# Optimization experiments

Measured on AMD Instinct MI355X. Metric: run time of the kernel, lower is better.

The kernel has to match this reference:

```python
import jax, jax.numpy as jnp
import numpy as np

B, W, S, D, H = 16, 128, 16, 768, 12
HD = D // H

def _ln(x, g, b):
    m = x.mean(-1, keepdims=True)
    v = ((x - m) ** 2).mean(-1, keepdims=True)
    return (x - m) / jnp.sqrt(v + 1e-5) * g + b

def _lin(x, w, b):
    return x @ w.T + b

def _rope(t):
    # t: (N, H, L, HD); interleaved even/odd rotation, base 10000
    inv = 1.0 / (10000.0 ** (jnp.arange(0, HD, 2, dtype=jnp.float32) / HD))
    fr = jnp.arange(t.shape[2], dtype=jnp.float32)[:, None] * inv[None, :]  # (L, HD//2)
    cos, sin = jnp.cos(fr), jnp.sin(fr)
    te, to = t[..., ::2], t[..., 1::2]
    return jnp.stack([te * cos - to * sin, te * sin + to * cos], -1).reshape(t.shape)

def _mha(q, k, v, mask=None):
    # q,k,v: (N, H, L, HD)
    s = jnp.einsum('nhqd,nhkd->nhqk', q, k) / jnp.sqrt(jnp.float32(HD))
    if mask is not None:
        s = jnp.where(mask[None, None], -jnp.inf, s)
    a = jax.nn.softmax(s, axis=-1)
    return jnp.einsum('nhqk,nhkd->nhqd', a, v)

def _heads(t, L):
    return t.reshape(-1, L, H, HD).transpose(0, 2, 1, 3)

def setup_inputs() -> dict:
    key = jax.random.key(0)
    ks = jax.random.split(key, 16)
    def w(i, shape):
        return jax.random.normal(ks[i], shape, jnp.float32) * 0.02
    return {
        'x': jax.random.normal(ks[0], (B, W, S, D), jnp.float32),
        'causal_mask': jnp.triu(jnp.ones((W, W), dtype=bool), k=1),
        'sn_g': jnp.ones((D,), jnp.float32), 'sn_b': jnp.zeros((D,), jnp.float32),
        'sa_in_w': w(1, (3 * D, D)), 'sa_in_b': jnp.zeros((3 * D,), jnp.float32),
        'sa_out_w': w(2, (D, D)), 'sa_out_b': jnp.zeros((D,), jnp.float32),
        'tn_g': jnp.ones((D,), jnp.float32), 'tn_b': jnp.zeros((D,), jnp.float32),
        'tq_w': w(3, (D, D)), 'tq_b': jnp.zeros((D,), jnp.float32),
        'tk_w': w(4, (D, D)), 'tk_b': jnp.zeros((D,), jnp.float32),
        'tv_w': w(5, (D, D)), 'tv_b': jnp.zeros((D,), jnp.float32),
        'to_w': w(6, (D, D)), 'to_b': jnp.zeros((D,), jnp.float32),
        'fn_g': jnp.ones((D,), jnp.float32), 'fn_b': jnp.zeros((D,), jnp.float32),
        'f1_w': w(7, (4 * D, D)), 'f1_b': jnp.zeros((4 * D,), jnp.float32),
        'f2_w': w(8, (D, 4 * D)), 'f2_b': jnp.zeros((D,), jnp.float32),
    }

def reference(x, causal_mask, sn_g, sn_b, sa_in_w, sa_in_b, sa_out_w, sa_out_b,
              tn_g, tn_b, tq_w, tq_b, tk_w, tk_b, tv_w, tv_b, to_w, to_b,
              fn_g, fn_b, f1_w, f1_b, f2_w, f2_b):
    # ---- spatial attention within each timestep: (B*W, S, D) ----
    xs = x.reshape(B * W, S, D)
    xn = _ln(xs, sn_g, sn_b)
    q, k, v = jnp.split(_lin(xn, sa_in_w, sa_in_b), 3, axis=-1)
    o = _mha(_heads(q, S), _heads(k, S), _heads(v, S))
    o = o.transpose(0, 2, 1, 3).reshape(B * W, S, D)
    xs = xs + _lin(o, sa_out_w, sa_out_b)
    x = xs.reshape(B, W, S, D)
    # ---- causal temporal attention with RoPE: (B*S, W, D) ----
    xt = x.transpose(0, 2, 1, 3).reshape(B * S, W, D)
    xn = _ln(xt, tn_g, tn_b)
    q = _rope(_heads(_lin(xn, tq_w, tq_b), W))
    k = _rope(_heads(_lin(xn, tk_w, tk_b), W))
    v = _heads(_lin(xn, tv_w, tv_b), W)
    o = _mha(q, k, v, causal_mask)
    o = o.transpose(0, 2, 1, 3).reshape(B * S, W, D)
    xt = xt + _lin(o, to_w, to_b)
    x = xt.reshape(B, S, W, D).transpose(0, 2, 1, 3)
    # ---- feed-forward (exact GELU, as torch default) ----
    h = jax.nn.gelu(_lin(_ln(x, fn_g, fn_b), f1_w, f1_b), approximate=False)
    return x + _lin(h, f2_w, f2_b)
```

## Files before the change

### kernel.cpp

```cpp
#include <hip/hip_runtime.h>
#include <stdint.h>


#define NB 16
#define NW 128
#define NS 16
#define ND 768
#define NH 12
#define NTOK 32768

typedef __attribute__((ext_vector_type(8))) short short8;
typedef __attribute__((ext_vector_type(4))) float f32x4;

__device__ __forceinline__ float blo(unsigned v){ return __builtin_bit_cast(float, v << 16); }
__device__ __forceinline__ float bhi(unsigned v){ return __builtin_bit_cast(float, v & 0xffff0000u); }
__device__ __forceinline__ float bus(unsigned short u){ return __builtin_bit_cast(float, ((unsigned)u) << 16); }
__device__ __forceinline__ unsigned short f2b(float f){
  unsigned u = __builtin_bit_cast(unsigned, f);
  u += 0x7fffu + ((u >> 16) & 1u);
  return (unsigned short)(u >> 16);
}
__device__ __forceinline__ void gld_lds16(const void* g, void* l){
  __builtin_amdgcn_global_load_lds((const __attribute__((address_space(1))) void*)g,
                                   (__attribute__((address_space(3))) void*)l, 16, 0, 0);
}

__global__ __launch_bounds__(256) void convert_k(const float* __restrict__ in,
                                                 unsigned short* __restrict__ out, int n4){
  int i = blockIdx.x * 256 + threadIdx.x;
  int stride = gridDim.x * 256;
  for (; i < n4; i += stride){
    float4 v = ((const float4*)in)[i];
    unsigned lo = (unsigned)f2b(v.x) | ((unsigned)f2b(v.y) << 16);
    unsigned hi = (unsigned)f2b(v.z) | ((unsigned)f2b(v.w) << 16);
    ((uint2*)out)[i] = make_uint2(lo, hi);
  }
}

__global__ __launch_bounds__(256) void concat3_k(const float* __restrict__ a, const float* __restrict__ b,
                                                 const float* __restrict__ c, float* __restrict__ o){
  int i = blockIdx.x * 256 + threadIdx.x;
  if (i < 768){ o[i] = a[i]; o[768 + i] = b[i]; o[1536 + i] = c[i]; }
}

__global__ __launch_bounds__(256) void rope_k(float* __restrict__ tab){
  int i = blockIdx.x * 256 + threadIdx.x;
  if (i < 128 * 32){
    int w = i >> 5, p = i & 31;
    float inv = powf(10000.0f, -((float)(2 * p)) / 64.0f);
    float ang = (float)w * inv;
    tab[i * 2] = cosf(ang);
    tab[i * 2 + 1] = sinf(ang);
  }
}

template<int INF32>
__global__ __launch_bounds__(256) void ln_k(const void* __restrict__ xin, const float* __restrict__ g,
                                            const float* __restrict__ bt, unsigned short* __restrict__ out){
  const int row = blockIdx.x;
  const int t = threadIdx.x;
  const float* xf = (const float*)xin;
  const unsigned short* xb = (const unsigned short*)xin;
  float v[3];
#pragma unroll
  for (int i = 0; i < 3; ++i){
    int j = t + i * 256;
    v[i] = INF32 ? xf[(size_t)row * 768 + j] : bus(xb[(size_t)row * 768 + j]);
  }
  float s = v[0] + v[1] + v[2];
  float ss = v[0]*v[0] + v[1]*v[1] + v[2]*v[2];
#pragma unroll
  for (int o = 1; o < 64; o <<= 1){ s += __shfl_xor(s, o, 64); ss += __shfl_xor(ss, o, 64); }
  __shared__ float red[8];
  int w = t >> 6;
  if ((t & 63) == 0){ red[w*2] = s; red[w*2+1] = ss; }
  __syncthreads();
  s = red[0] + red[2] + red[4] + red[6];
  ss = red[1] + red[3] + red[5] + red[7];
  float mean = s * (1.0f / 768.0f);
  float var = ss * (1.0f / 768.0f) - mean * mean;
  float rstd = rsqrtf(var + 1e-5f);
#pragma unroll
  for (int i = 0; i < 3; ++i){
    int j = t + i * 256;
    out[(size_t)row * 768 + j] = f2b((v[i] - mean) * rstd * g[j] + bt[j]);
  }
}

template<int MODE, int MROWS>
__global__ __launch_bounds__(512) void gemm256_k(const unsigned short* __restrict__ A,
                                                 const unsigned short* __restrict__ Bw,
                                                 const float* __restrict__ bias,
                                                 const void* __restrict__ resid,
                                                 void* __restrict__ outp, int K, int M){
  constexpr int MH = MROWS / 2;
  constexpr int ASH = (MROWS == 8) ? 14 : 13;
  constexpr int NJA = MROWS / 4;
  constexpr int LDSZ = 4 * (1 << ASH) + 65536;
  __shared__ char LB[LDSZ];
  char* const Asl = LB;
  char* const Bsl = LB + 4 * (1 << ASH);
  const int tid = threadIdx.x;
  const int lane = tid & 63, w = tid >> 6;
  const int llo = lane & 15, lhi = lane >> 4;
  const int wm = w >> 2, wn = w & 3;
  const int NT = K >> 6;

  const int gx = gridDim.x;
  const int nwg = gx * gridDim.y;
  const int orig = blockIdx.y * gx + blockIdx.x;
  const int lin = (nwg & 7) ? orig : ((orig & 7) * (nwg >> 3) + (orig >> 3));
  const int by = lin / gx, bx = lin - by * gx;
  const int brow = by * (MROWS << 5);
  const int bcol = bx << 8;

  const int r0 = tid >> 3, cp = tid & 7;
  const int swz = (cp << 4) ^ ((r0 & 7) << 4);
  const char* aG = (const char*)(A + (size_t)(brow + r0) * K) + swz;
  const char* bG = (const char*)(Bw + (size_t)(bcol + r0) * K) + swz;
  const int J  = K * 128;
  const int Ha = K * (MROWS << 5);
  const int Hb = K * 256;
  const int ldst = w << 10;

  auto stage_a = [&](int gb, char* slotbase){
    gld_lds16(aG + gb, slotbase + ldst);
    if constexpr (NJA == 2) gld_lds16(aG + gb + J, slotbase + ldst + (1 << 13));
  };
  auto stage_b = [&](int gb, char* slotbase){
    gld_lds16(bG + gb, slotbase + ldst);
    gld_lds16(bG + gb + J, slotbase + ldst + (1 << 13));
  };

  stage_a(0,        Asl);
  stage_a(Ha,       Asl + (1 << ASH));
  stage_b(0,        Bsl);
  stage_b(Hb,       Bsl + (1 << 14));
  stage_a(128,      Asl + (2 << ASH));
  stage_a(128 + Ha, Asl + (3 << ASH));
  if constexpr (NJA == 2) asm volatile("s_waitcnt vmcnt(4)" ::: "memory");
  else                    asm volatile("s_waitcnt vmcnt(2)" ::: "memory");
  __builtin_amdgcn_s_barrier();

  f32x4 acc[MROWS][4];
#pragma unroll
  for (int m = 0; m < MROWS; ++m)
#pragma unroll
    for (int n = 0; n < 4; ++n) acc[m][n] = f32x4{0.f, 0.f, 0.f, 0.f};

  for (int t = 0; t < NT; ++t){
    const char* Ab = Asl + (((2 * t + wm) & 3) << ASH);
    const char* Bb = Bsl + (((2 * t + (wn >> 1)) & 3) << 14);
    const int tb = t << 7;
    short8 a0[MH][2], a1[MH][2], b0[2][2], b1[2][2];

#pragma unroll
    for (int ni = 0; ni < 2; ++ni){
      const int cc = ((wn & 1) << 6) + (ni << 4) + llo;
#pragma unroll
      for (int ks = 0; ks < 2; ++ks)
        b0[ni][ks] = *(const short8*)(Bb + cc * 128 + (((ks << 6) + (lhi << 4)) ^ ((cc & 7) << 4)));
    }
#pragma unroll
    for (int mi = 0; mi < MH; ++mi){
      const int rr = (mi << 4) + llo;
#pragma unroll
      for (int ks = 0; ks < 2; ++ks)
        a0[mi][ks] = *(const short8*)(Ab + rr * 128 + (((ks << 6) + (lhi << 4)) ^ ((rr & 7) << 4)));
    }
    if (t + 1 < NT) stage_b(tb + 128, Bsl + (((2 * t + 2) & 3) << 14));
    __builtin_amdgcn_s_barrier();
    __builtin_amdgcn_s_setprio(1);
#pragma unroll
    for (int mi = 0; mi < MH; ++mi)
#pragma unroll
      for (int ni = 0; ni < 2; ++ni){
        acc[mi][ni] = __builtin_amdgcn_mfma_f32_16x16x32_bf16(b0[ni][0], a0[mi][0], acc[mi][ni], 0, 0, 0);
        acc[mi][ni] = __builtin_amdgcn_mfma_f32_16x16x32_bf16(b0[ni][1], a0[mi][1], acc[mi][ni], 0, 0, 0);
      }
    __builtin_amdgcn_s_setprio(0);
    __builtin_amdgcn_s_barrier();

#pragma unroll
    for (int mi = 0; mi < MH; ++mi){
      const int rr = (MH << 4) + (mi << 4) + llo;
#pragma unroll
      for (int ks = 0; ks < 2; ++ks)
        a1[mi][ks] = *(const short8*)(Ab + rr * 128 + (((ks << 6) + (lhi << 4)) ^ ((rr & 7) << 4)));
    }
#pragma unroll
    for (int ni = 0; ni < 2; ++ni){
      const int cc = ((wn & 1) << 6) + 32 + (ni << 4) + llo;
#pragma unroll
      for (int ks = 0; ks < 2; ++ks)
        b1[ni][ks] = *(const short8*)(Bb + cc * 128 + (((ks << 6) + (lhi << 4)) ^ ((cc & 7) << 4)));
    }
    if (t + 1 < NT) stage_b(tb + 128 + Hb, Bsl + (((2 * t + 3) & 3) << 14));
    __builtin_amdgcn_s_barrier();
    __builtin_amdgcn_s_setprio(1);
#pragma unroll
    for (int mi = 0; mi < MH; ++mi)
#pragma unroll
      for (int ni = 0; ni < 2; ++ni){
        acc[MH + mi][ni] = __builtin_amdgcn_mfma_f32_16x16x32_bf16(b0[ni][0], a1[mi][0], acc[MH + mi][ni], 0, 0, 0);
        acc[MH + mi][ni] = __builtin_amdgcn_mfma_f32_16x16x32_bf16(b0[ni][1], a1[mi][1], acc[MH + mi][ni], 0, 0, 0);
      }
    __builtin_amdgcn_s_setprio(0);
    __builtin_amdgcn_s_barrier();

    if (t + 2 < NT) stage_a(tb + 256, Asl + (((2 * t + 4) & 3) << ASH));
    __builtin_amdgcn_s_barrier();
    __builtin_amdgcn_s_setprio(1);
#pragma unroll
    for (int mi = 0; mi < MH; ++mi)
#pragma unroll
      for (int ni = 0; ni < 2; ++ni){
        acc[mi][2 + ni] = __builtin_amdgcn_mfma_f32_16x16x32_bf16(b1[ni][0], a0[mi][0], acc[mi][2 + ni], 0, 0, 0);
        acc[mi][2 + ni] = __builtin_amdgcn_mfma_f32_16x16x32_bf16(b1[ni][1], a0[mi][1], acc[mi][2 + ni], 0, 0, 0);
      }
    __builtin_amdgcn_s_setprio(0);
    __builtin_amdgcn_s_barrier();

    if (t + 2 < NT) stage_a(tb + 256 + Ha, Asl + (((2 * t + 5) & 3) << ASH));
    __builtin_amdgcn_s_barrier();
    __builtin_amdgcn_s_setprio(1);
#pragma unroll
    for (int mi = 0; mi < MH; ++mi)
#pragma unroll
      for (int ni = 0; ni < 2; ++ni){
        acc[MH + mi][2 + ni] = __builtin_amdgcn_mfma_f32_16x16x32_bf16(b1[ni][0], a1[mi][0], acc[MH + mi][2 + ni], 0, 0, 0);
        acc[MH + mi][2 + ni] = __builtin_amdgcn_mfma_f32_16x16x32_bf16(b1[ni][1], a1[mi][1], acc[MH + mi][2 + ni], 0, 0, 0);
      }
    __builtin_amdgcn_s_setprio(0);
    if (t + 2 < NT){
      if constexpr (NJA == 2) asm volatile("s_waitcnt vmcnt(4)" ::: "memory");
      else                    asm volatile("s_waitcnt vmcnt(2)" ::: "memory");
    } else {
      asm volatile("s_waitcnt vmcnt(0)" ::: "memory");
    }
    __builtin_amdgcn_s_barrier();
  }

  const int orow = brow + wm * (MROWS << 4);
  const int ocol = bcol + (wn << 6);
  const unsigned short* resb = (const unsigned short*)resid;
  const float* resf = (const float*)resid;
#pragma unroll
  for (int m = 0; m < MROWS; ++m){
    const int row = orow + (m << 4) + llo;
    const size_t rb = (size_t)row * M;
#pragma unroll
    for (int n = 0; n < 4; ++n){
      const int col = ocol + (n << 4) + (lhi << 2);
      const float4 bv = *(const float4*)&bias[col];
      float v0 = acc[m][n][0] + bv.x;
      float v1 = acc[m][n][1] + bv.y;
      float v2 = acc[m][n][2] + bv.z;
      float v3 = acc[m][n][3] + bv.w;
      const size_t off = rb + col;
      if (MODE == 1){
        float y0 = v0 * (1.5957691216f + 0.0713548163f * v0 * v0);
        float y1 = v1 * (1.5957691216f + 0.0713548163f * v1 * v1);
        float y2 = v2 * (1.5957691216f + 0.0713548163f * v2 * v2);
        float y3 = v3 * (1.5957691216f + 0.0713548163f * v3 * v3);
        v0 = v0 / (1.0f + __expf(-y0));
        v1 = v1 / (1.0f + __expf(-y1));
        v2 = v2 / (1.0f + __expf(-y2));
        v3 = v3 / (1.0f + __expf(-y3));
      } else if (MODE == 2){
        const float4 rv = *(const float4*)&resf[off];
        v0 += rv.x; v1 += rv.y; v2 += rv.z; v3 += rv.w;
      } else if (MODE == 3 || MODE == 4){
        const uint2 rv = *(const uint2*)&resb[off];
        v0 += blo(rv.x); v1 += bhi(rv.x); v2 += blo(rv.y); v3 += bhi(rv.y);
      }
      if (MODE == 4){
        float4 ov; ov.x = v0; ov.y = v1; ov.z = v2; ov.w = v3;
        *(float4*)&((float*)outp)[off] = ov;
      } else {
        unsigned lo = (unsigned)f2b(v0) | ((unsigned)f2b(v1) << 16);
        unsigned hi = (unsigned)f2b(v2) | ((unsigned)f2b(v3) << 16);
        *(uint2*)&((unsigned short*)outp)[off] = make_uint2(lo, hi);
      }
    }
  }
}

__global__ __launch_bounds__(256) void sattn_k(const unsigned short* __restrict__ qkv,
                                               unsigned short* __restrict__ o){
  const int bw = blockIdx.x, h = blockIdx.y;
  const int t = threadIdx.x;
  __shared__ unsigned short qh[16 * 68], kh[16 * 68], vh[16 * 68];
  __shared__ float pl[16 * 17];
  const int row = t >> 4, c4 = t & 15;
  const size_t base = ((size_t)(bw * 16 + row)) * 2304 + h * 64 + c4 * 4;
  *(uint2*)&qh[row * 68 + c4 * 4] = *(const uint2*)&qkv[base];
  *(uint2*)&kh[row * 68 + c4 * 4] = *(const uint2*)&qkv[base + 768];
  *(uint2*)&vh[row * 68 + c4 * 4] = *(const uint2*)&qkv[base + 1536];
  __syncthreads();

  const int q = row, k = c4;
  float s = 0.f;
#pragma unroll
  for (int c = 0; c < 16; ++c){
    uint2 qv = *(const uint2*)&qh[q * 68 + c * 4];
    uint2 kv = *(const uint2*)&kh[k * 68 + c * 4];
    s += blo(qv.x) * blo(kv.x) + bhi(qv.x) * bhi(kv.x);
    s += blo(qv.y) * blo(kv.y) + bhi(qv.y) * bhi(kv.y);
  }
  s *= 0.125f;
  float m = s;
#pragma unroll
  for (int off = 1; off < 16; off <<= 1) m = fmaxf(m, __shfl_xor(m, off, 64));
  float p = __expf(s - m);
  float su = p;
#pragma unroll
  for (int off = 1; off < 16; off <<= 1) su += __shfl_xor(su, off, 64);
  pl[q * 17 + k] = p / su;
  __syncthreads();

  float o0 = 0.f, o1 = 0.f, o2 = 0.f, o3 = 0.f;
#pragma unroll
  for (int kk = 0; kk < 16; ++kk){
    float pw = pl[q * 17 + kk];
    uint2 vv = *(const uint2*)&vh[kk * 68 + c4 * 4];
    o0 += pw * blo(vv.x); o1 += pw * bhi(vv.x);
    o2 += pw * blo(vv.y); o3 += pw * bhi(vv.y);
  }
  const size_t ob = ((size_t)(bw * 16 + q)) * 768 + h * 64 + c4 * 4;
  unsigned r0 = (unsigned)f2b(o0) | ((unsigned)f2b(o1) << 16);
  unsigned r1 = (unsigned)f2b(o2) | ((unsigned)f2b(o3) << 16);
  *(uint2*)&o[ob] = make_uint2(r0, r1);
}

__global__ __launch_bounds__(256) void tattn_k(const unsigned short* __restrict__ qkv,
                                               const float* __restrict__ rope,
                                               unsigned short* __restrict__ o){
  const int bs = blockIdx.x, h = blockIdx.y;
  const int b = bs >> 4, s = bs & 15;
  const int t = threadIdx.x, lane = t & 63, w = t >> 6;
  const int lhi = lane >> 4, llo = lane & 15;
  __shared__ unsigned short Qs[128 * 64];
  __shared__ unsigned short Ks[128 * 64];
  __shared__ unsigned short Vt[64 * 128];
  __shared__ unsigned short P[128 * 128];

  {
    const int r = t >> 1;
    const int dbase = (t & 1) * 32;
    const size_t tokb = ((size_t)((b * 128 + r) * 16 + s)) * 2304 + h * 64;
    const float2* rp = (const float2*)rope;
#pragma unroll
    for (int mch = 0; mch < 4; ++mch){
      const int d0 = dbase + mch * 8;
      uint4 qv = *(const uint4*)&qkv[tokb + d0];
      uint4 kv = *(const uint4*)&qkv[tokb + 768 + d0];
      uint4 vv = *(const uint4*)&qkv[tokb + 1536 + d0];
      unsigned qin[4] = {qv.x, qv.y, qv.z, qv.w};
      unsigned kin[4] = {kv.x, kv.y, kv.z, kv.w};
      unsigned qo[4], ko[4];
#pragma unroll
      for (int j = 0; j < 4; ++j){
        float2 cssn = rp[r * 32 + (d0 >> 1) + j];
        float cs = cssn.x, sn = cssn.y;
        float qe = blo(qin[j]), qd = bhi(qin[j]);
        float ke = blo(kin[j]), kd = bhi(kin[j]);
        qo[j] = (unsigned)f2b(qe * cs - qd * sn) | ((unsigned)f2b(qe * sn + qd * cs) << 16);
        ko[j] = (unsigned)f2b(ke * cs - kd * sn) | ((unsigned)f2b(ke * sn + kd * cs) << 16);
      }
      const int byq = r * 128 + ((d0 * 2) ^ ((r & 7) << 4));
      *(uint4*)((char*)Qs + byq) = make_uint4(qo[0], qo[1], qo[2], qo[3]);
      *(uint4*)((char*)Ks + byq) = make_uint4(ko[0], ko[1], ko[2], ko[3]);
      unsigned vin[4] = {vv.x, vv.y, vv.z, vv.w};
#pragma unroll
      for (int j = 0; j < 8; ++j){
        const int d = d0 + j;
        unsigned short val = (j & 1) ? (unsigned short)(vin[j >> 1] >> 16)
                                     : (unsigned short)(vin[j >> 1] & 0xffffu);
        *(unsigned short*)((char*)Vt + d * 256 + ((r * 2) ^ ((d & 7) << 4))) = val;
      }
    }
  }
  __syncthreads();

  const int qbase = w * 32;
  f32x4 st[8][2];
#pragma unroll
  for (int i = 0; i < 8; ++i){ st[i][0] = f32x4{0.f,0.f,0.f,0.f}; st[i][1] = f32x4{0.f,0.f,0.f,0.f}; }
#pragma unroll
  for (int kd = 0; kd < 2; ++kd){
    short8 bq[2];
#pragma unroll
    for (int fq = 0; fq < 2; ++fq){
      const int qr = qbase + fq * 16 + llo;
      bq[fq] = *(const short8*)((const char*)Qs + qr * 128 + ((kd * 64 + lhi * 16) ^ ((qr & 7) << 4)));
    }
#pragma unroll
    for (int fk = 0; fk < 8; ++fk){
      const int kr = fk * 16 + llo;
      short8 ak = *(const short8*)((const char*)Ks + kr * 128 + ((kd * 64 + lhi * 16) ^ ((kr & 7) << 4)));
      st[fk][0] = __builtin_amdgcn_mfma_f32_16x16x32_bf16(ak, bq[0], st[fk][0], 0, 0, 0);
      st[fk][1] = __builtin_amdgcn_mfma_f32_16x16x32_bf16(ak, bq[1], st[fk][1], 0, 0, 0);
    }
  }

#pragma unroll
  for (int fq = 0; fq < 2; ++fq){
    const int qg = qbase + fq * 16 + llo;
    float m = -1e30f;
#pragma unroll
    for (int fk = 0; fk < 8; ++fk)
#pragma unroll
      for (int rr = 0; rr < 4; ++rr){
        const int kg = fk * 16 + lhi * 4 + rr;
        float sv = (kg <= qg) ? st[fk][fq][rr] : -1e30f;
        st[fk][fq][rr] = sv;
        m = fmaxf(m, sv);
      }
    m = fmaxf(m, __shfl_xor(m, 16, 64));
    m = fmaxf(m, __shfl_xor(m, 32, 64));
    float su = 0.f;
#pragma unroll
    for (int fk = 0; fk < 8; ++fk)
#pragma unroll
      for (int rr = 0; rr < 4; ++rr){
        float p = __expf((st[fk][fq][rr] - m) * 0.125f);
        st[fk][fq][rr] = p;
        su += p;
      }
    su += __shfl_xor(su, 16, 64);
    su += __shfl_xor(su, 32, 64);
    const float rs = 1.0f / su;
#pragma unroll
    for (int fk = 0; fk < 8; ++fk){
      const int kk = fk * 16 + lhi * 4;
      unsigned lo = (unsigned)f2b(st[fk][fq][0] * rs) | ((unsigned)f2b(st[fk][fq][1] * rs) << 16);
      unsigned hi = (unsigned)f2b(st[fk][fq][2] * rs) | ((unsigned)f2b(st[fk][fq][3] * rs) << 16);
      *(uint2*)((char*)P + qg * 256 + ((kk * 2) ^ ((qg & 7) << 4))) = make_uint2(lo, hi);
    }
  }
  __syncthreads();

  f32x4 oacc[2][4];
#pragma unroll
  for (int i = 0; i < 2; ++i)
#pragma unroll
    for (int j = 0; j < 4; ++j) oacc[i][j] = f32x4{0.f,0.f,0.f,0.f};
#pragma unroll
  for (int ks = 0; ks < 4; ++ks){
    short8 pa[2];
#pragma unroll
    for (int fq = 0; fq < 2; ++fq){
      const int qr = qbase + fq * 16 + llo;
      pa[fq] = *(const short8*)((const char*)P + qr * 256 + ((ks * 64 + lhi * 16) ^ ((qr & 7) << 4)));
    }
#pragma unroll
    for (int fd = 0; fd < 4; ++fd){
      const int dr = fd * 16 + llo;
      short8 vb = *(const short8*)((const char*)Vt + dr * 256 + ((ks * 64 + lhi * 16) ^ ((dr & 7) << 4)));
      oacc[0][fd] = __builtin_amdgcn_mfma_f32_16x16x32_bf16(pa[0], vb, oacc[0][fd], 0, 0, 0);
      oacc[1][fd] = __builtin_amdgcn_mfma_f32_16x16x32_bf16(pa[1], vb, oacc[1][fd], 0, 0, 0);
    }
  }

#pragma unroll
  for (int fq = 0; fq < 2; ++fq)
#pragma unroll
    for (int fd = 0; fd < 4; ++fd)
#pragma unroll
      for (int rr = 0; rr < 4; ++rr){
        const int qg = qbase + fq * 16 + lhi * 4 + rr;
        const int d = fd * 16 + llo;
        const size_t ob = ((size_t)((b * 128 + qg) * 16 + s)) * 768 + h * 64 + d;
        o[ob] = f2b(oacc[fq][fd][rr]);
      }
}

__global__ __launch_bounds__(256) void sentinel_k(float* out){
  if (blockIdx.x == 0 && threadIdx.x == 0) out[0] = 12345.0f;
}

extern "C" void kernel_launch(void* const* d_in, const int* in_sizes, int n_in,
                              void* d_out, int out_size, void* d_ws, size_t ws_size,
                              hipStream_t stream){
  const float* x       = (const float*)d_in[0];
  const float* sn_g    = (const float*)d_in[2];
  const float* sn_b    = (const float*)d_in[3];
  const float* sa_in_w = (const float*)d_in[4];
  const float* sa_in_b = (const float*)d_in[5];
  const float* sa_out_w= (const float*)d_in[6];
  const float* sa_out_b= (const float*)d_in[7];
  const float* tn_g    = (const float*)d_in[8];
  const float* tn_b    = (const float*)d_in[9];
  const float* tq_w    = (const float*)d_in[10];
  const float* tq_b    = (const float*)d_in[11];
  const float* tk_w    = (const float*)d_in[12];
  const float* tk_b    = (const float*)d_in[13];
  const float* tv_w    = (const float*)d_in[14];
  const float* tv_b    = (const float*)d_in[15];
  const float* to_w    = (const float*)d_in[16];
  const float* to_b    = (const float*)d_in[17];
  const float* fn_g    = (const float*)d_in[18];
  const float* fn_b    = (const float*)d_in[19];
  const float* f1_w    = (const float*)d_in[20];
  const float* f1_b    = (const float*)d_in[21];
  const float* f2_w    = (const float*)d_in[22];
  const float* f2_b    = (const float*)d_in[23];

  char* ws = (char*)d_ws;
  size_t off = 0;
  auto alloc = [&](size_t bytes) -> void* {
    void* p = ws + off;
    off += (bytes + 255) & ~(size_t)255;
    return p;
  };
  unsigned short* Wqkv = (unsigned short*)alloc((size_t)2304*768*2);
  unsigned short* Wo1  = (unsigned short*)alloc((size_t)768*768*2);
  unsigned short* W3   = (unsigned short*)alloc((size_t)2304*768*2);
  float*          b3   = (float*)alloc(2304*4);
  unsigned short* Wto  = (unsigned short*)alloc((size_t)768*768*2);
  unsigned short* Wf1  = (unsigned short*)alloc((size_t)3072*768*2);
  unsigned short* Wf2  = (unsigned short*)alloc((size_t)768*3072*2);
  float*          rope = (float*)alloc(128*32*2*4);
  unsigned short* xn   = (unsigned short*)alloc((size_t)NTOK*768*2);
  unsigned short* qkv  = (unsigned short*)alloc((size_t)NTOK*3072*2);
  unsigned short* xs2  = (unsigned short*)alloc((size_t)NTOK*768*2);
  unsigned short* xt2  = (unsigned short*)alloc((size_t)NTOK*768*2);
  unsigned short* ob   = xn;

  if (ws_size < off){ sentinel_k<<<1, 64, 0, stream>>>((float*)d_out); return; }

  convert_k<<<1024, 256, 0, stream>>>(sa_in_w, Wqkv, 2304*768/4);
  convert_k<<<512, 256, 0, stream>>>(sa_out_w, Wo1, 768*768/4);
  convert_k<<<512, 256, 0, stream>>>(tq_w, W3, 768*768/4);
  convert_k<<<512, 256, 0, stream>>>(tk_w, W3 + 768*768, 768*768/4);
  convert_k<<<512, 256, 0, stream>>>(tv_w, W3 + 2*768*768, 768*768/4);
  concat3_k<<<3, 256, 0, stream>>>(tq_b, tk_b, tv_b, b3);
  convert_k<<<512, 256, 0, stream>>>(to_w, Wto, 768*768/4);
  convert_k<<<1024, 256, 0, stream>>>(f1_w, Wf1, 3072*768/4);
  convert_k<<<1024, 256, 0, stream>>>(f2_w, Wf2, 768*3072/4);
  rope_k<<<16, 256, 0, stream>>>(rope);

  ln_k<1><<<NTOK, 256, 0, stream>>>(x, sn_g, sn_b, xn);
  gemm256_k<0,4><<<dim3(9, 256), 512, 0, stream>>>(xn, Wqkv, sa_in_b, nullptr, qkv, 768, 2304);
  sattn_k<<<dim3(2048, 12), 256, 0, stream>>>(qkv, ob);
  gemm256_k<2,4><<<dim3(3, 256), 512, 0, stream>>>(ob, Wo1, sa_out_b, x, xs2, 768, 768);

  ln_k<0><<<NTOK, 256, 0, stream>>>(xs2, tn_g, tn_b, xn);
  gemm256_k<0,4><<<dim3(9, 256), 512, 0, stream>>>(xn, W3, b3, nullptr, qkv, 768, 2304);
  tattn_k<<<dim3(256, 12), 256, 0, stream>>>(qkv, rope, ob);
  gemm256_k<3,4><<<dim3(3, 256), 512, 0, stream>>>(ob, Wto, to_b, xs2, xt2, 768, 768);

  ln_k<0><<<NTOK, 256, 0, stream>>>(xt2, fn_g, fn_b, xn);
  gemm256_k<1,8><<<dim3(12, 128), 512, 0, stream>>>(xn, Wf1, f1_b, nullptr, qkv, 768, 3072);
  gemm256_k<4,4><<<dim3(3, 256), 512, 0, stream>>>(qkv, Wf2, f2_b, xt2, d_out, 3072, 768);
}
```

Before: 1.129 ms.

## Prefetch next k-tile fragments from LDS and reorder GEMM phase schedule

Restructures the GEMM main loop so the a0/b0 register fragments for the next k-step are read from LDS before the last MFMA quadrant of the current step, and the a1/b1 reads are interleaved with earlier quadrants. The aim is to hide LDS read latency behind MFMA work and to drop one barrier phase per iteration. The cost is that the fragment registers now live across the loop, which raises register pressure, and the changed barrier and waitcnt ordering risks LDS slot hazards if any reuse window is wrong.

```diff
diff --git a/kernel.cpp b/kernel.cpp
--- a/kernel.cpp
+++ b/kernel.cpp
@@ -132,6 +132,44 @@
     gld_lds16(bG + gb + J, slotbase + ldst + (1 << 13));
   };
 
+  short8 a0[MH][2], a1[MH][2], b0[2][2], b1[2][2];
+  auto rd_a = [&](short8 (&dst)[MH][2], const char* Ab, int rbase){
+#pragma unroll
+    for (int mi = 0; mi < MH; ++mi){
+      const int rr = rbase + (mi << 4) + llo;
+#pragma unroll
+      for (int ks = 0; ks < 2; ++ks)
+        dst[mi][ks] = *(const short8*)(Ab + rr * 128 + (((ks << 6) + (lhi << 4)) ^ ((rr & 7) << 4)));
+    }
+  };
+  auto rd_b = [&](short8 (&dst)[2][2], const char* Bb, int cbase){
+#pragma unroll
+    for (int ni = 0; ni < 2; ++ni){
+      const int cc = cbase + (ni << 4) + llo;
+#pragma unroll
+      for (int ks = 0; ks < 2; ++ks)
+        dst[ni][ks] = *(const short8*)(Bb + cc * 128 + (((ks << 6) + (lhi << 4)) ^ ((cc & 7) << 4)));
+    }
+  };
+
+  f32x4 acc[MROWS][4];
+#pragma unroll
+  for (int m = 0; m < MROWS; ++m)
+#pragma unroll
+    for (int n = 0; n < 4; ++n) acc[m][n] = f32x4{0.f, 0.f, 0.f, 0.f};
+
+  auto mfma_q = [&](int mo, int no, short8 (&bb)[2][2], short8 (&aa)[MH][2]){
+    __builtin_amdgcn_s_setprio(1);
+#pragma unroll
+    for (int mi = 0; mi < MH; ++mi)
+#pragma unroll
+      for (int ni = 0; ni < 2; ++ni){
+        acc[mo + mi][no + ni] = __builtin_amdgcn_mfma_f32_16x16x32_bf16(bb[ni][0], aa[mi][0], acc[mo + mi][no + ni], 0, 0, 0);
+        acc[mo + mi][no + ni] = __builtin_amdgcn_mfma_f32_16x16x32_bf16(bb[ni][1], aa[mi][1], acc[mo + mi][no + ni], 0, 0, 0);
+      }
+    __builtin_amdgcn_s_setprio(0);
+  };
+
   stage_a(0,        Asl);
   stage_a(Ha,       Asl + (1 << ASH));
   stage_b(0,        Bsl);
@@ -141,103 +179,50 @@
   if constexpr (NJA == 2) asm volatile("s_waitcnt vmcnt(4)" ::: "memory");
   else                    asm volatile("s_waitcnt vmcnt(2)" ::: "memory");
   __builtin_amdgcn_s_barrier();
-
-  f32x4 acc[MROWS][4];
-#pragma unroll
-  for (int m = 0; m < MROWS; ++m)
-#pragma unroll
-    for (int n = 0; n < 4; ++n) acc[m][n] = f32x4{0.f, 0.f, 0.f, 0.f};
+  {
+    const char* Ab0 = Asl + ((wm & 3) << ASH);
+    const char* Bb0 = Bsl + (((wn >> 1) & 3) << 14);
+    rd_b(b0, Bb0, (wn & 1) << 6);
+    rd_a(a0, Ab0, 0);
+  }
 
   for (int t = 0; t < NT; ++t){
     const char* Ab = Asl + (((2 * t + wm) & 3) << ASH);
     const char* Bb = Bsl + (((2 * t + (wn >> 1)) & 3) << 14);
     const int tb = t << 7;
-    short8 a0[MH][2], a1[MH][2], b0[2][2], b1[2][2];
-
-#pragma unroll
-    for (int ni = 0; ni < 2; ++ni){
-      const int cc = ((wn & 1) << 6) + (ni << 4) + llo;
-#pragma unroll
-      for (int ks = 0; ks < 2; ++ks)
-        b0[ni][ks] = *(const short8*)(Bb + cc * 128 + (((ks << 6) + (lhi << 4)) ^ ((cc & 7) << 4)));
-    }
-#pragma unroll
-    for (int mi = 0; mi < MH; ++mi){
-      const int rr = (mi << 4) + llo;
-#pragma unroll
-      for (int ks = 0; ks < 2; ++ks)
-        a0[mi][ks] = *(const short8*)(Ab + rr * 128 + (((ks << 6) + (lhi << 4)) ^ ((rr & 7) << 4)));
-    }
+
+    rd_a(a1, Ab, MH << 4);
+    __builtin_amdgcn_s_barrier();
+    mfma_q(0, 0, b0, a0);
+    __builtin_amdgcn_s_barrier();
+
+    rd_b(b1, Bb, ((wn & 1) << 6) + 32);
     if (t + 1 < NT) stage_b(tb + 128, Bsl + (((2 * t + 2) & 3) << 14));
     __builtin_amdgcn_s_barrier();
-    __builtin_amdgcn_s_setprio(1);
-#pragma unroll
-    for (int mi = 0; mi < MH; ++mi)
-#pragma unroll
-      for (int ni = 0; ni < 2; ++ni){
-        acc[mi][ni] = __builtin_amdgcn_mfma_f32_16x16x32_bf16(b0[ni][0], a0[mi][0], acc[mi][ni], 0, 0, 0);
-        acc[mi][ni] = __builtin_amdgcn_mfma_f32_16x16x32_bf16(b0[ni][1], a0[mi][1], acc[mi][ni], 0, 0, 0);
-      }
-    __builtin_amdgcn_s_setprio(0);
-    __builtin_amdgcn_s_barrier();
-
-#pragma unroll
-    for (int mi = 0; mi < MH; ++mi){
-      const int rr = (MH << 4) + (mi << 4) + llo;
-#pragma unroll
-      for (int ks = 0; ks < 2; ++ks)
-        a1[mi][ks] = *(const short8*)(Ab + rr * 128 + (((ks << 6) + (lhi << 4)) ^ ((rr & 7) << 4)));
-    }
-#pragma unroll
-    for (int ni = 0; ni < 2; ++ni){
-      const int cc = ((wn & 1) << 6) + 32 + (ni << 4) + llo;
-#pragma unroll
-      for (int ks = 0; ks < 2; ++ks)
-        b1[ni][ks] = *(const short8*)(Bb + cc * 128 + (((ks << 6) + (lhi << 4)) ^ ((cc & 7) << 4)));
-    }
+    mfma_q(MH, 0, b0, a1);
+    __builtin_amdgcn_s_barrier();
+
     if (t + 1 < NT) stage_b(tb + 128 + Hb, Bsl + (((2 * t + 3) & 3) << 14));
-    __builtin_amdgcn_s_barrier();
-    __builtin_amdgcn_s_setprio(1);
-#pragma unroll
-    for (int mi = 0; mi < MH; ++mi)
-#pragma unroll
-      for (int ni = 0; ni < 2; ++ni){
-        acc[MH + mi][ni] = __builtin_amdgcn_mfma_f32_16x16x32_bf16(b0[ni][0], a1[mi][0], acc[MH + mi][ni], 0, 0, 0);
-        acc[MH + mi][ni] = __builtin_amdgcn_mfma_f32_16x16x32_bf16(b0[ni][1], a1[mi][1], acc[MH + mi][ni], 0, 0, 0);
-      }
-    __builtin_amdgcn_s_setprio(0);
-    __builtin_amdgcn_s_barrier();
-
     if (t + 2 < NT) stage_a(tb + 256, Asl + (((2 * t + 4) & 3) << ASH));
     __builtin_amdgcn_s_barrier();
-    __builtin_amdgcn_s_setprio(1);
-#pragma unroll
-    for (int mi = 0; mi < MH; ++mi)
-#pragma unroll
-      for (int ni = 0; ni < 2; ++ni){
-        acc[mi][2 + ni] = __builtin_amdgcn_mfma_f32_16x16x32_bf16(b1[ni][0], a0[mi][0], acc[mi][2 + ni], 0, 0, 0);
-        acc[mi][2 + ni] = __builtin_amdgcn_mfma_f32_16x16x32_bf16(b1[ni][1], a0[mi][1], acc[mi][2 + ni], 0, 0, 0);
-      }
-    __builtin_amdgcn_s_setprio(0);
-    __builtin_amdgcn_s_barrier();
-
-    if (t + 2 < NT) stage_a(tb + 256 + Ha, Asl + (((2 * t + 5) & 3) << ASH));
-    __builtin_amdgcn_s_barrier();
-    __builtin_amdgcn_s_setprio(1);
-#pragma unroll
-    for (int mi = 0; mi < MH; ++mi)
-#pragma unroll
-      for (int ni = 0; ni < 2; ++ni){
-        acc[MH + mi][2 + ni] = __builtin_amdgcn_mfma_f32_16x16x32_bf16(b1[ni][0], a1[mi][0], acc[MH + mi][2 + ni], 0, 0, 0);
-        acc[MH + mi][2 + ni] = __builtin_amdgcn_mfma_f32_16x16x32_bf16(b1[ni][1], a1[mi][1], acc[MH + mi][2 + ni], 0, 0, 0);
-      }
-    __builtin_amdgcn_s_setprio(0);
+    mfma_q(0, 2, b1, a0);
+    __builtin_amdgcn_s_barrier();
+
     if (t + 2 < NT){
+      stage_a(tb + 256 + Ha, Asl + (((2 * t + 5) & 3) << ASH));
       if constexpr (NJA == 2) asm volatile("s_waitcnt vmcnt(4)" ::: "memory");
       else                    asm volatile("s_waitcnt vmcnt(2)" ::: "memory");
     } else {
       asm volatile("s_waitcnt vmcnt(0)" ::: "memory");
     }
+    __builtin_amdgcn_s_barrier();
+    if (t + 1 < NT){
+      const char* Abn = Asl + (((2 * t + 2 + wm) & 3) << ASH);
+      const char* Bbn = Bsl + (((2 * t + 2 + (wn >> 1)) & 3) << 14);
+      rd_b(b0, Bbn, (wn & 1) << 6);
+      rd_a(a0, Abn, 0);
+    }
+    mfma_q(MH, 2, b1, a1);
     __builtin_amdgcn_s_barrier();
   }
 
```

Measured after the change: 1.176 ms. +4.1%, slower.
